# Optimization experiments

Hardware: AMD Instinct MI355X
Metric: run time of the kernel (lower is better)

Reference implementation:

```python
import jax, jax.numpy as jnp
import numpy as np
from jax import lax

B, C, H, W = 32, 256, 56, 56

def _conv(x, w, stride, groups=1, pad='VALID'):
    return lax.conv_general_dilated(x, w, (stride, stride), pad,
                                    feature_group_count=groups,
                                    dimension_numbers=('NCHW', 'OIHW', 'NCHW'))

def _ln(x, g, b, eps=1e-5):
    mu = jnp.mean(x, -1, keepdims=True)
    var = jnp.mean((x - mu) ** 2, -1, keepdims=True)
    return (x - mu) * lax.rsqrt(var + eps) * g + b

def setup_inputs() -> dict:
    key = jax.random.key(0)
    ks = jax.random.split(key, 16)
    s = 0.02
    Ch = C // 2
    d = {}
    d['x'] = jax.random.normal(ks[0], (B, C, H, W), jnp.float32)
    d['Wq'] = jax.random.normal(ks[1], (C, C), jnp.float32) * s;  d['bq'] = jnp.zeros((C,), jnp.float32)
    d['Wk'] = jax.random.normal(ks[2], (C, C), jnp.float32) * s;  d['bk'] = jnp.zeros((C,), jnp.float32)
    d['Wv'] = jax.random.normal(ks[3], (C, C), jnp.float32) * s;  d['bv'] = jnp.zeros((C,), jnp.float32)
    d['sr1_w'] = jax.random.normal(ks[4], (C, C, 8, 8), jnp.float32) * s; d['sr1_b'] = jnp.zeros((C,), jnp.float32)
    d['ln1_g'] = jnp.ones((C,), jnp.float32); d['ln1_b'] = jnp.zeros((C,), jnp.float32)
    d['sr2_w'] = jax.random.normal(ks[5], (C, C, 4, 4), jnp.float32) * s; d['sr2_b'] = jnp.zeros((C,), jnp.float32)
    d['ln2_g'] = jnp.ones((C,), jnp.float32); d['ln2_b'] = jnp.zeros((C,), jnp.float32)
    d['Wkv1'] = jax.random.normal(ks[6], (C, C), jnp.float32) * s; d['bkv1'] = jnp.zeros((C,), jnp.float32)
    d['Wkv2'] = jax.random.normal(ks[7], (C, C), jnp.float32) * s; d['bkv2'] = jnp.zeros((C,), jnp.float32)
    d['lc1_w'] = jax.random.normal(ks[8], (Ch, 1, 3, 3), jnp.float32) * s; d['lc1_b'] = jnp.zeros((Ch,), jnp.float32)
    d['lc2_w'] = jax.random.normal(ks[9], (Ch, 1, 3, 3), jnp.float32) * s; d['lc2_b'] = jnp.zeros((Ch,), jnp.float32)
    d['rp_w'] = jax.random.normal(ks[10], (C, C), jnp.float32) * s;  d['rp_b'] = jnp.zeros((C,), jnp.float32)
    d['rp12_w'] = jax.random.normal(ks[11], (C, C), jnp.float32) * s; d['rp12_b'] = jnp.zeros((C,), jnp.float32)
    d['dw_w'] = jax.random.normal(ks[12], (C, 2), jnp.float32) * 0.5  # Conv3d (2,1,1) depthwise, no bias
    return d

def reference(x, Wq, bq, Wk, bk, Wv, bv, sr1_w, sr1_b, ln1_g, ln1_b,
              sr2_w, sr2_b, ln2_g, ln2_b, Wkv1, bkv1, Wkv2, bkv2,
              lc1_w, lc1_b, lc2_w, lc2_b, rp_w, rp_b, rp12_w, rp12_b, dw_w):
    Bx, Cc, h, w = x.shape
    N = h * w
    Ch = Cc // 2
    xt = x.reshape(Bx, Cc, N).transpose(0, 2, 1)                 # [B,N,C]
    q = jax.nn.softmax(xt @ Wq + bq, axis=-1)                    # softmax over channels
    q1, q2 = q[..., :Ch], q[..., Ch:]

    # spatial-reduction branches (conv -> LN -> GELU)
    x1 = _conv(x, sr1_w, 8) + sr1_b[:, None, None]               # [B,C,7,7]
    x1 = jax.nn.gelu(_ln(x1.reshape(Bx, Cc, -1).transpose(0, 2, 1), ln1_g, ln1_b), approximate=False)
    x2 = _conv(x, sr2_w, 4) + sr2_b[:, None, None]               # [B,C,14,14]
    x2 = jax.nn.gelu(_ln(x2.reshape(Bx, Cc, -1).transpose(0, 2, 1), ln2_g, ln2_b), approximate=False)

    def branch(xr, Wkv, bkv, lc_w, lc_b, qh, hh):
        kv = (xr @ Wkv + bkv).reshape(Bx, -1, 2, Ch)
        k = jax.nn.softmax(kv[:, :, 0], axis=1)                  # softmax over reduced tokens
        v = kv[:, :, 1]
        vsp = v.transpose(0, 2, 1).reshape(Bx, Ch, hh, hh)
        v = v + (_conv(vsp, lc_w, 1, groups=Ch, pad='SAME') + lc_b[:, None, None]).reshape(Bx, Ch, -1).transpose(0, 2, 1)
        ctx = jnp.einsum('bnk,bnv->bkv', k, v)                   # [B,Ch,Ch]
        return jnp.einsum('bnk,bkv->bnv', qh, ctx)               # [B,N,Ch]

    a1 = branch(x1, Wkv1, bkv1, lc1_w, lc1_b, q1, 7)
    a2 = branch(x2, Wkv2, bkv2, lc2_w, lc2_b, q2, 14)
    eff2 = jnp.concatenate([a1, a2], axis=-1)                    # [B,N,C]
    eff2 = jnp.einsum('bni,oi->bon', eff2, rp12_w).reshape(Bx, Cc, h, w) + rp12_b[None, :, None, None]

    # global efficient-attention branch
    keys = jax.nn.softmax(xt @ Wk + bk, axis=1)                  # softmax over tokens
    values = xt @ Wv + bv
    ctx = jnp.einsum('bnk,bnv->bkv', keys, values)               # [B,C,C]
    att = jnp.einsum('bnk,bkv->bnv', q, ctx)                     # [B,N,C]
    eff = jnp.einsum('bni,oi->bon', att, rp_w).reshape(Bx, Cc, h, w) + rp_b[None, :, None, None]

    # Conv3d (2,1,1) depthwise merge over the two branches
    out = eff * dw_w[:, 0][None, :, None, None] + eff2 * dw_w[:, 1][None, :, None, None]
    return out
```

## Files before the change

### kernel.cpp

```cpp
#include <hip/hip_runtime.h>
#include <hip/hip_bf16.h>
#include <math.h>

#define B_ 32
#define H_ 56
#define W_ 56
#define N_ 3136
#define NT_ 100352

typedef short short8 __attribute__((ext_vector_type(8)));
typedef float f32x4 __attribute__((ext_vector_type(4)));

__device__ __forceinline__ unsigned short f2b(float f){
  union { float f; unsigned u; } v; v.f = f;
  return (unsigned short)((v.u + 0x7FFFu + ((v.u>>16)&1u)) >> 16);
}

#define LDSW(row, bo) ((unsigned)((row)*128 + ((bo) ^ (((row)&7)<<4))))

__device__ __forceinline__ short8 ldfrag(const char* base, int row, int kk){
  return *(const short8*)(base + LDSW(row, kk*2));
}
__device__ __forceinline__ f32x4 mfma16(short8 a, short8 b, f32x4 c){
  return __builtin_amdgcn_mfma_f32_16x16x32_bf16(a, b, c, 0, 0, 0);
}

__device__ __forceinline__ void gld16(void* lds, const void* g){
  __builtin_amdgcn_global_load_lds((__attribute__((address_space(1))) void*)g,
                                   (__attribute__((address_space(3))) void*)lds,
                                   16, 0, 0);
}

__global__ void prep_kernel(const float* __restrict__ Wq, const float* __restrict__ Wk,
                            const float* __restrict__ Wv, const float* __restrict__ Wkv1,
                            const float* __restrict__ Wkv2, const float* __restrict__ sr1w,
                            const float* __restrict__ sr2w, const float* __restrict__ rpw,
                            const float* __restrict__ rpb, const float* __restrict__ rp12w,
                            const float* __restrict__ rp12b, const float* __restrict__ dww,
                            unsigned short* WqT, unsigned short* WkT, unsigned short* WvT,
                            unsigned short* Wkv1T, unsigned short* Wkv2T,
                            unsigned short* srw1, unsigned short* srw2,
                            unsigned short* Acomb, float* bias_out)
{
  int idx = blockIdx.x*256 + threadIdx.x;
  const int total = 5*65536 + 4194304 + 1048576 + 131072 + 256;
  for (int i = idx; i < total; i += gridDim.x*256) {
    int j = i;
    if (j < 5*65536) {
      int w = j >> 16, e = j & 65535;
      int o = e >> 8, c = e & 255;
      const float* src = (w==0)?Wq:(w==1)?Wk:(w==2)?Wv:(w==3)?Wkv1:Wkv2;
      unsigned short* dst = (w==0)?WqT:(w==1)?WkT:(w==2)?WvT:(w==3)?Wkv1T:Wkv2T;
      dst[o*256+c] = f2b(src[c*256+o]);
      continue;
    }
    j -= 5*65536;
    if (j < 4194304) {
      int o = j >> 14, rem = j & 16383, pos = rem >> 8, c = rem & 255;
      srw1[j] = f2b(sr1w[o*16384 + c*64 + pos]);
      continue;
    }
    j -= 4194304;
    if (j < 1048576) {
      int o = j >> 12, rem = j & 4095, pos = rem >> 8, c = rem & 255;
      srw2[j] = f2b(sr2w[o*4096 + c*16 + pos]);
      continue;
    }
    j -= 1048576;
    if (j < 131072) {
      int o = j >> 9, i2 = j & 511;
      float v = (i2 < 256) ? dww[o*2+0]*rpw[o*256+i2]
                           : dww[o*2+1]*rp12w[o*256+(i2-256)];
      Acomb[o*512+i2] = f2b(v);
      continue;
    }
    j -= 131072;
    bias_out[j] = dww[j*2+0]*rpb[j] + dww[j*2+1]*rp12b[j];
  }
}

__global__ void transpose_kernel(const float* __restrict__ x, unsigned short* __restrict__ xt)
{
  __shared__ float tile[64][65];
  int bn = blockIdx.x; int b = bn / 49; int n0 = (bn - b*49)*64;
  int c0 = blockIdx.y*64;
  int t = threadIdx.x;
  {
    int cl = t >> 2, nq = t & 3;
    const float* src = x + ((size_t)(b*256 + c0 + cl))*N_ + n0 + nq*16;
#pragma unroll
    for (int j = 0; j < 4; j++){
      float4 v = *(const float4*)(src + j*4);
      tile[cl][nq*16 + j*4 + 0] = v.x;
      tile[cl][nq*16 + j*4 + 1] = v.y;
      tile[cl][nq*16 + j*4 + 2] = v.z;
      tile[cl][nq*16 + j*4 + 3] = v.w;
    }
  }
  __syncthreads();
  {
    int nl = t >> 2, cq = t & 3;
    unsigned short pk[16];
#pragma unroll
    for (int j=0;j<16;j++) pk[j] = f2b(tile[cq*16+j][nl]);
    unsigned short* dst = xt + ((size_t)(b*N_ + n0 + nl))*256 + c0 + cq*16;
    *(uint4*)dst = *(uint4*)&pk[0];
    *(uint4*)(dst+8) = *(uint4*)&pk[8];
  }
}

__global__ __launch_bounds__(256,2) void qkv3_kernel(
    const unsigned short* __restrict__ xt,
    const unsigned short* __restrict__ WqT, const unsigned short* __restrict__ WkT,
    const unsigned short* __restrict__ WvT,
    const float* __restrict__ bq, const float* __restrict__ bk, const float* __restrict__ bv,
    unsigned short* __restrict__ qbuf, unsigned short* __restrict__ KexpT,
    unsigned short* __restrict__ VT, float* __restrict__ s_q, float* __restrict__ s_k)
{
  __shared__ __align__(16) char smem[32768 + 32768 + 1024];
  char* At = smem;
  char* Bt = smem + 32768;
  float* redbuf = (float*)(smem + 65536);
  const int t = threadIdx.x, wave = t>>6, lane = t&63, l15 = lane&15, l4 = lane>>4;
  const int r0 = blockIdx.x*64;
  const int b = r0 / N_;
  const int nl0 = r0 - b*N_;

#pragma unroll
  for (int c4=0;c4<4;c4++)
#pragma unroll
    for (int j=0;j<2;j++){
      int chunk = j*256 + t; int row = chunk>>3, c8 = chunk&7;
      int c8s = c8 ^ (row&7);
      gld16(At + c4*8192 + (j*256 + wave*64)*16,
            xt + (size_t)(r0+row)*256 + c4*64 + c8s*8);
    }
  __syncthreads();

  for (int mat=0; mat<3; mat++){
    const unsigned short* BT = (mat==0)?WqT:(mat==1)?WkT:WvT;
    const float* bias = (mat==0)?bq:(mat==1)?bk:bv;
    const f32x4 vzero = {0.f,0.f,0.f,0.f};
    f32x4 acc[4][4];
#pragma unroll
    for (int i=0;i<4;i++)
#pragma unroll
      for (int j=0;j<4;j++) acc[i][j] = vzero;

    for (int k0c=0;k0c<4;k0c++){
#pragma unroll
      for (int j=0;j<8;j++){
        int chunk = j*256 + t; int row = chunk>>3, c8 = chunk&7;
        int c8s = c8 ^ (row&7);
        gld16(Bt + (j*256 + wave*64)*16, BT + (size_t)row*256 + k0c*64 + c8s*8);
      }
      __syncthreads();
#pragma unroll
      for (int ks=0;ks<2;ks++){
        short8 af[4], bfr[4];
#pragma unroll
        for (int mi=0;mi<4;mi++) af[mi]  = ldfrag(At + k0c*8192, mi*16 + l15, ks*32 + l4*8);
#pragma unroll
        for (int ni=0;ni<4;ni++) bfr[ni] = ldfrag(Bt, wave*64 + ni*16 + l15, ks*32 + l4*8);
#pragma unroll
        for (int mi=0;mi<4;mi++)
#pragma unroll
          for (int ni=0;ni<4;ni++)
            acc[mi][ni] = mfma16(af[mi], bfr[ni], acc[mi][ni]);
      }
      __syncthreads();
    }

    float bb4[4];
#pragma unroll
    for (int ni=0;ni<4;ni++) bb4[ni] = bias[wave*64 + ni*16 + l15];

    if (mat == 0) {
      float rs[4][4];
#pragma unroll
      for (int mi=0;mi<4;mi++)
#pragma unroll
        for (int r=0;r<4;r++) rs[mi][r] = 0.f;
#pragma unroll
      for (int mi=0;mi<4;mi++)
#pragma unroll
        for (int ni=0;ni<4;ni++)
#pragma unroll
          for (int r=0;r<4;r++){
            float e = __expf(acc[mi][ni][r] + bb4[ni]);
            acc[mi][ni][r] = e;
            rs[mi][r] += e;
          }
#pragma unroll
      for (int mi=0;mi<4;mi++)
#pragma unroll
        for (int r=0;r<4;r++){
          float s = rs[mi][r];
          s += __shfl_xor(s, 1); s += __shfl_xor(s, 2);
          s += __shfl_xor(s, 4); s += __shfl_xor(s, 8);
          rs[mi][r] = s;
        }
      if (l15 == 0){
#pragma unroll
        for (int mi=0;mi<4;mi++)
#pragma unroll
          for (int r=0;r<4;r++)
            redbuf[wave*64 + mi*16 + l4*4 + r] = rs[mi][r];
      }
      __syncthreads();
      unsigned short* qb = (unsigned short*)Bt;
#pragma unroll
      for (int mi=0;mi<4;mi++)
#pragma unroll
        for (int r=0;r<4;r++){
          int rr = mi*16 + l4*4 + r;
#pragma unroll
          for (int ni=0;ni<4;ni++)
            qb[rr*256 + wave*64 + ni*16 + l15] = f2b(acc[mi][ni][r]);
        }
      if (t < 64){
        s_q[r0 + t] = redbuf[t] + redbuf[64+t] + redbuf[128+t] + redbuf[192+t];
      }
      __syncthreads();
#pragma unroll
      for (int j=0;j<8;j++){
        int chunk = j*256 + t;
        int row = chunk >> 5, c8 = chunk & 31;
        *(uint4*)(qbuf + (size_t)(r0+row)*256 + c8*8) = *(const uint4*)(qb + row*256 + c8*8);
      }
      __syncthreads();
    } else {
      float cs[4] = {0.f,0.f,0.f,0.f};
#pragma unroll
      for (int mi=0;mi<4;mi++)
#pragma unroll
        for (int ni=0;ni<4;ni++)
#pragma unroll
          for (int r=0;r<4;r++){
            float v = acc[mi][ni][r] + bb4[ni];
            if (mat == 1){ v = __expf(v); cs[ni] += v; }
            int row = mi*16 + l4*4 + r;
            int col = wave*64 + ni*16 + l15;
            *(unsigned short*)(Bt + LDSW(col, row*2)) = f2b(v);
          }
      if (mat == 1){
#pragma unroll
        for (int ni=0;ni<4;ni++){
          float s = cs[ni];
          s += __shfl_xor(s, 16);
          s += __shfl_xor(s, 32);
          if (lane < 16) atomicAdd(&s_k[b*256 + wave*64 + ni*16 + lane], s);
        }
      }
      __syncthreads();
      unsigned short* ot = (mat==1) ? KexpT : VT;
#pragma unroll
      for (int j=0;j<8;j++){
        int chunk = j*256 + t;
        int c = chunk >> 3, n8 = chunk & 7;
        *(uint4*)(ot + ((size_t)b*256 + c)*N_ + nl0 + n8*8) = *(const uint4*)(Bt + LDSW(c, n8*16));
      }
      __syncthreads();
    }
  }
}

template<int MODE>
__global__ __launch_bounds__(256,2) void tile128_kernel(
    const unsigned short* __restrict__ Ag, const unsigned short* __restrict__ Bg,
    unsigned short* __restrict__ outg, float* __restrict__ part)
{
  __shared__ __align__(16) char smem[32768];
  char* At = smem; char* Bt = smem + 16384;
  const int b = blockIdx.x;
  const int mt = (MODE==0) ? (blockIdx.y >> 1) : blockIdx.y;
  const int nt = (MODE==0) ? (blockIdx.y & 1)  : blockIdx.z;
  const int it0 = (MODE==0) ? blockIdx.z*7 : 0;
  const int it1 = (MODE==0) ? it0+7 : 8;
  const int t = threadIdx.x;
  const int wave = t>>6, lane = t&63, l15 = lane&15, l4 = lane>>4;
  const int wm = (wave>>1)*64, wn = (wave&1)*64;
  const size_t astr = (MODE==0) ? (size_t)N_ : (size_t)512;
  const unsigned short* A  = (MODE==0) ? (Ag + ((size_t)b*256 + mt*128)*N_) : (Ag + (size_t)mt*128*512);
  const unsigned short* Bv = (MODE==0) ? (Bg + ((size_t)b*256 + nt*128)*N_) : (Bg + ((size_t)b*256 + nt*128)*512);
  const f32x4 vzero = {0.f,0.f,0.f,0.f};
  f32x4 acc[4][4];
#pragma unroll
  for (int i=0;i<4;i++)
#pragma unroll
    for (int j=0;j<4;j++) acc[i][j] = vzero;

  for (int it=it0; it<it1; it++){
    const int k0 = it*64;
#pragma unroll
    for (int j=0;j<4;j++){
      int chunk = j*256 + t; int row = chunk>>3, c8 = chunk&7;
      int c8s = c8 ^ (row&7);
      gld16(At + (j*256 + wave*64)*16, A + (size_t)row*astr + k0 + c8s*8);
    }
#pragma unroll
    for (int j=0;j<4;j++){
      int chunk = j*256 + t; int row = chunk>>3, c8 = chunk&7;
      int c8s = c8 ^ (row&7);
      gld16(Bt + (j*256 + wave*64)*16, Bv + (size_t)row*astr + k0 + c8s*8);
    }
    __syncthreads();
#pragma unroll
    for (int ks=0;ks<2;ks++){
      short8 af[4], bfr[4];
#pragma unroll
      for (int mi=0;mi<4;mi++) af[mi]  = ldfrag(At, wm + mi*16 + l15, ks*32 + l4*8);
#pragma unroll
      for (int ni=0;ni<4;ni++) bfr[ni] = ldfrag(Bt, wn + ni*16 + l15, ks*32 + l4*8);
#pragma unroll
      for (int mi=0;mi<4;mi++)
#pragma unroll
        for (int ni=0;ni<4;ni++)
          acc[mi][ni] = mfma16(af[mi], bfr[ni], acc[mi][ni]);
    }
    __syncthreads();
  }
  if (MODE==0){
    const int sk = blockIdx.z;
#pragma unroll
    for (int mi=0;mi<4;mi++)
#pragma unroll
      for (int r=0;r<4;r++){
        int kg = mt*128 + wm + mi*16 + l4*4 + r;
        size_t basep = (((size_t)sk*B_ + b)*256 + kg)*256 + nt*128 + wn;
#pragma unroll
        for (int ni=0;ni<4;ni++)
          part[basep + ni*16 + l15] = acc[mi][ni][r];
      }
  } else {
#pragma unroll
    for (int mi=0;mi<4;mi++)
#pragma unroll
      for (int r=0;r<4;r++){
        int og = mt*128 + wm + mi*16 + l4*4 + r;
#pragma unroll
        for (int ni=0;ni<4;ni++)
          outg[(size_t)b*65536 + (size_t)og*256 + nt*128 + wn + ni*16 + l15] = f2b(acc[mi][ni][r]);
      }
  }
}

__global__ __launch_bounds__(256) void ctxred_kernel(
    const float* __restrict__ part, const float* __restrict__ s_k,
    unsigned short* __restrict__ ctxcomb)
{
  int e = (blockIdx.x*256 + threadIdx.x)*4;
  int b = e >> 16; int rem = e & 65535; int kg = rem >> 8; int col = rem & 255;
  float4 s = {0.f,0.f,0.f,0.f};
#pragma unroll
  for (int sk=0; sk<7; sk++){
    float4 p = *(const float4*)(part + ((((size_t)sk*B_ + b)*256 + kg)<<8) + col);
    s.x += p.x; s.y += p.y; s.z += p.z; s.w += p.w;
  }
  float inv = 1.0f / s_k[b*256 + kg];
  unsigned short pk[4] = {f2b(s.x*inv), f2b(s.y*inv), f2b(s.z*inv), f2b(s.w*inv)};
  *(uint2*)(ctxcomb + ((size_t)b*256 + kg)*512 + col) = *(uint2*)&pk[0];
}

template<int S, int OW, int KW, int NSK, int MPB, int KTOT>
__device__ __forceinline__ void srconv_body(
    const unsigned short* __restrict__ xt, const unsigned short* __restrict__ wbf,
    float* __restrict__ part, int bid, char* At, char* Bt)
{
  const int KCH = KTOT / NSK;
  const int Mtot = B_*MPB;
  const int sk = bid % NSK, tile = bid / NSK;
  const int t = threadIdx.x, wave = t>>6, lane = t&63, l15 = lane&15, l4 = lane>>4;
  const f32x4 vzero = {0.f,0.f,0.f,0.f};
  f32x4 acc[4][4];
#pragma unroll
  for (int i=0;i<4;i++)
#pragma unroll
    for (int j=0;j<4;j++) acc[i][j] = vzero;

  size_t abase[2];
#pragma unroll
  for (int j=0;j<2;j++){
    int chunk = j*256 + t;
    int row = chunk >> 3, c8 = chunk & 7;
    int c8s = c8 ^ (row&7);
    int rowc = tile*64 + row; if (rowc > Mtot-1) rowc = Mtot-1;
    int b = rowc / MPB; int m = rowc - b*MPB;
    int p = m / OW; int q = m - p*OW;
    abase[j] = ((size_t)b*N_ + (size_t)(S*p)*W_ + S*q)*256 + c8s*8;
  }

  for (int kt = 0; kt < KCH; kt += 64){
    const int k0 = sk*KCH + kt;
    const int pos = k0 >> 8, cc = k0 & 255;
    const int dy = pos / KW, dx = pos - dy*KW;
    const size_t off = (size_t)(dy*W_ + dx)*256 + cc;
#pragma unroll
    for (int j=0;j<2;j++){
      gld16(At + (j*256 + wave*64)*16, xt + abase[j] + off);
    }
#pragma unroll
    for (int j=0;j<8;j++){
      int chunk = j*256 + t; int row = chunk>>3, c8 = chunk&7;
      int c8s = c8 ^ (row&7);
      gld16(Bt + (j*256 + wave*64)*16, wbf + (size_t)row*KTOT + k0 + c8s*8);
    }
    __syncthreads();
#pragma unroll
    for (int ks=0;ks<2;ks++){
      short8 af[4], bfr[4];
#pragma unroll
      for (int mi=0;mi<4;mi++) af[mi]  = ldfrag(At, mi*16 + l15, ks*32 + l4*8);
#pragma unroll
      for (int ni=0;ni<4;ni++) bfr[ni] = ldfrag(Bt, wave*64 + ni*16 + l15, ks*32 + l4*8);
#pragma unroll
      for (int mi=0;mi<4;mi++)
#pragma unroll
        for (int ni=0;ni<4;ni++)
          acc[mi][ni] = mfma16(af[mi], bfr[ni], acc[mi][ni]);
    }
    __syncthreads();
  }
#pragma unroll
  for (int mi=0;mi<4;mi++)
#pragma unroll
    for (int r=0;r<4;r++){
      int row = tile*64 + mi*16 + l4*4 + r;
      if (row < Mtot){
        size_t basep = ((size_t)sk*Mtot + row)*256;
#pragma unroll
        for (int ni=0;ni<4;ni++)
          part[basep + wave*64 + ni*16 + l15] = acc[mi][ni][r];
      }
    }
}

__global__ __launch_bounds__(256,4) void srconv_both_kernel(
    const unsigned short* __restrict__ xt, const unsigned short* __restrict__ srw1,
    const unsigned short* __restrict__ srw2, float* __restrict__ x1part,
    float* __restrict__ x2part)
{
  __shared__ __align__(16) char smem[8192 + 32768];
  if (blockIdx.x < 392)
    srconv_body<4,14,4,4,196,4096>(xt, srw2, x2part, blockIdx.x, smem, smem+8192);
  else
    srconv_body<8,7,8,32,49,16384>(xt, srw1, x1part, blockIdx.x-392, smem, smem+8192);
}

__device__ __forceinline__ void lngelu_body(
    const float* __restrict__ part, const float* __restrict__ srb,
    const float* __restrict__ g, const float* __restrict__ bb,
    unsigned short* __restrict__ out, int M, int nsk, int Mtot, int bid,
    float* red)
{
  int b = bid / M, m = bid - b*M;
  int c = threadIdx.x;
  float v = srb[c];
  for (int s=0;s<nsk;s++) v += part[((size_t)s*Mtot + b*M + m)*256 + c];
  int wave = c>>6, lane = c&63;
  float s1 = v;
  s1 += __shfl_xor(s1,1); s1 += __shfl_xor(s1,2); s1 += __shfl_xor(s1,4);
  s1 += __shfl_xor(s1,8); s1 += __shfl_xor(s1,16); s1 += __shfl_xor(s1,32);
  if (lane==0) red[wave] = s1;
  __syncthreads();
  float mu = (red[0]+red[1]+red[2]+red[3]) * (1.0f/256.0f);
  float d = v - mu;
  float s2 = d*d;
  s2 += __shfl_xor(s2,1); s2 += __shfl_xor(s2,2); s2 += __shfl_xor(s2,4);
  s2 += __shfl_xor(s2,8); s2 += __shfl_xor(s2,16); s2 += __shfl_xor(s2,32);
  if (lane==0) red[4+wave] = s2;
  __syncthreads();
  float var = (red[4]+red[5]+red[6]+red[7]) * (1.0f/256.0f);
  float y = d * rsqrtf(var + 1e-5f) * g[c] + bb[c];
  float ge = 0.5f * y * (1.0f + erff(y * 0.70710678118654752f));
  out[((size_t)b*M + m)*256 + c] = f2b(ge);
}

__global__ __launch_bounds__(256) void lngelu_both_kernel(
    const float* __restrict__ x1part, const float* __restrict__ x2part,
    const float* __restrict__ sr1b, const float* __restrict__ sr2b,
    const float* __restrict__ ln1g, const float* __restrict__ ln1b,
    const float* __restrict__ ln2g, const float* __restrict__ ln2b,
    unsigned short* __restrict__ x1g, unsigned short* __restrict__ x2g)
{
  __shared__ float red[8];
  if (blockIdx.x < 1568)
    lngelu_body(x1part, sr1b, ln1g, ln1b, x1g, 49, 32, 1568, blockIdx.x, red);
  else
    lngelu_body(x2part, sr2b, ln2g, ln2b, x2g, 196, 4, 6272, blockIdx.x-1568, red);
}

__global__ __launch_bounds__(256,2) void kv_both_kernel(
    const unsigned short* __restrict__ x1g, const unsigned short* __restrict__ Wkv1T,
    const float* __restrict__ bkv1, float* __restrict__ kexp1, float* __restrict__ vraw1,
    const unsigned short* __restrict__ x2g, const unsigned short* __restrict__ Wkv2T,
    const float* __restrict__ bkv2, float* __restrict__ kexp2, float* __restrict__ vraw2)
{
  __shared__ __align__(16) char smem[8192 + 32768];
  char* At = smem; char* Bt = smem + 8192;
  const unsigned short* A; const unsigned short* BT; const float* bias;
  float* kexp; float* vraw; int r0; int R;
  if (blockIdx.x < 25){ A=x1g; BT=Wkv1T; bias=bkv1; kexp=kexp1; vraw=vraw1; r0=blockIdx.x*64; R=1568; }
  else { A=x2g; BT=Wkv2T; bias=bkv2; kexp=kexp2; vraw=vraw2; r0=(blockIdx.x-25)*64; R=6272; }
  const int t = threadIdx.x, wave = t>>6, lane = t&63, l15 = lane&15, l4 = lane>>4;
  const f32x4 vzero = {0.f,0.f,0.f,0.f};
  f32x4 acc[4][4];
#pragma unroll
  for (int i=0;i<4;i++)
#pragma unroll
    for (int j=0;j<4;j++) acc[i][j] = vzero;

  for (int k0 = 0; k0 < 256; k0 += 64) {
#pragma unroll
    for (int j = 0; j < 2; j++){
      int chunk = j*256 + t;
      int row = chunk >> 3, c8 = chunk & 7;
      int c8s = c8 ^ (row&7);
      int rg = r0 + row; if (rg > R-1) rg = R-1;
      gld16(At + (j*256 + wave*64)*16, A + (size_t)rg*256 + k0 + c8s*8);
    }
#pragma unroll
    for (int j = 0; j < 8; j++){
      int chunk = j*256 + t;
      int row = chunk >> 3, c8 = chunk & 7;
      int c8s = c8 ^ (row&7);
      gld16(Bt + (j*256 + wave*64)*16, BT + (size_t)row*256 + k0 + c8s*8);
    }
    __syncthreads();
#pragma unroll
    for (int ks = 0; ks < 2; ks++){
      short8 af[4], bfr[4];
#pragma unroll
      for (int mi=0;mi<4;mi++) af[mi]  = ldfrag(At, mi*16 + l15, ks*32 + l4*8);
#pragma unroll
      for (int ni=0;ni<4;ni++) bfr[ni] = ldfrag(Bt, wave*64 + ni*16 + l15, ks*32 + l4*8);
#pragma unroll
      for (int mi=0;mi<4;mi++)
#pragma unroll
        for (int ni=0;ni<4;ni++)
          acc[mi][ni] = mfma16(af[mi], bfr[ni], acc[mi][ni]);
    }
    __syncthreads();
  }
  float bb4[4];
#pragma unroll
  for (int ni=0;ni<4;ni++) bb4[ni] = bias[wave*64 + ni*16 + l15];
#pragma unroll
  for (int mi=0;mi<4;mi++)
#pragma unroll
    for (int ni=0;ni<4;ni++)
#pragma unroll
      for (int r=0;r<4;r++){
        int rg = r0 + mi*16 + l4*4 + r;
        if (rg < R){
          int col = wave*64 + ni*16 + l15;
          float v = acc[mi][ni][r] + bb4[ni];
          if (col < 128) kexp[(size_t)rg*128 + col] = __expf(v);
          else           vraw[(size_t)rg*128 + (col-128)] = v;
        }
      }
}

__device__ __forceinline__ void dwconv_body(
    const float* __restrict__ vraw, const float* __restrict__ lcw,
    const float* __restrict__ lcb, float* __restrict__ vmod, int M, int OW, int idx)
{
  int ch = idx & 127; int rest = idx >> 7; int m = rest % M; int b = rest / M;
  if (b >= B_) return;
  int py = m / OW, px = m - py*OW;
  float acc = vraw[((size_t)b*M + m)*128 + ch] + lcb[ch];
#pragma unroll
  for (int dy=0;dy<3;dy++)
#pragma unroll
    for (int dx=0;dx<3;dx++){
      int yy = py+dy-1, xx = px+dx-1;
      if (yy>=0 && yy<OW && xx>=0 && xx<OW)
        acc += vraw[((size_t)b*M + yy*OW+xx)*128 + ch] * lcw[ch*9 + dy*3 + dx];
    }
  vmod[((size_t)b*M + m)*128 + ch] = acc;
}

__global__ __launch_bounds__(256) void dwconv_both_kernel(
    const float* __restrict__ vraw1, const float* __restrict__ lc1w,
    const float* __restrict__ lc1b, float* __restrict__ vmod1,
    const float* __restrict__ vraw2, const float* __restrict__ lc2w,
    const float* __restrict__ lc2b, float* __restrict__ vmod2)
{
  int gid = blockIdx.x*256 + threadIdx.x;
  if (blockIdx.x < 784) dwconv_body(vraw1, lc1w, lc1b, vmod1, 49, 7, gid);
  else dwconv_body(vraw2, lc2w, lc2b, vmod2, 196, 14, gid - 784*256);
}

__global__ __launch_bounds__(512) void ctxbr_both_kernel(
    const float* __restrict__ kexp1, const float* __restrict__ vmod1,
    const float* __restrict__ kexp2, const float* __restrict__ vmod2,
    unsigned short* __restrict__ ctxcomb)
{
  const int b = blockIdx.x;
  int kc = blockIdx.y;
  const float* kexp; const float* vmod; int M, BR;
  if (kc < 32){ kexp = kexp1; vmod = vmod1; M = 49; BR = 0; }
  else { kexp = kexp2; vmod = vmod2; M = 196; BR = 1; kc -= 32; }
  const int t = threadIdx.x;
  const int kl = t >> 7, j = t & 127;
  const int kk = kc*4 + kl;
  const float* kp = kexp + (size_t)b*M*128 + kk;
  const float* vp = vmod + (size_t)b*M*128 + j;
  float acc = 0.f, s = 0.f;
  for (int m = 0; m < M; m++){
    float kv = kp[(size_t)m*128];
    s += kv;
    acc += kv * vp[(size_t)m*128];
  }
  const int krow = BR ? (128+kk) : kk;
  unsigned short* dst = ctxcomb + ((size_t)b*256 + krow)*512;
  const int wbase = BR ? 384 : 256;
  const int zbase = BR ? 256 : 384;
  dst[wbase + j] = f2b(acc / s);
  dst[zbase + j] = 0;
}

__global__ __launch_bounds__(256,2) void final_kernel(
    const unsigned short* __restrict__ Gmat, const unsigned short* __restrict__ qbuf,
    const float* __restrict__ bias_out, const float* __restrict__ s_q,
    float* __restrict__ out)
{
  __shared__ __align__(16) char smem[16384 + 8192];
  char* At = smem; char* Bt = smem + 16384;
  const int b = blockIdx.x, ot = blockIdx.y, nt = blockIdx.z;
  const int t = threadIdx.x, wave = t>>6, lane = t&63, l15 = lane&15, l4 = lane>>4;
  const int wm = (wave>>1)*64, wn = (wave&1)*32;
  const unsigned short* A  = Gmat + ((size_t)b*256 + ot*128)*256;
  const unsigned short* Bq = qbuf + ((size_t)b*N_ + nt*64)*256;
  const f32x4 vzero = {0.f,0.f,0.f,0.f};
  f32x4 acc[4][2];
#pragma unroll
  for (int i=0;i<4;i++){ acc[i][0] = vzero; acc[i][1] = vzero; }

  for (int k0=0;k0<256;k0+=64){
#pragma unroll
    for (int j=0;j<4;j++){
      int chunk = j*256 + t; int row = chunk>>3, c8 = chunk&7;
      int c8s = c8 ^ (row&7);
      gld16(At + (j*256 + wave*64)*16, A + (size_t)row*256 + k0 + c8s*8);
    }
#pragma unroll
    for (int j=0;j<2;j++){
      int chunk = j*256 + t; int row = chunk>>3, c8 = chunk&7;
      int c8s = c8 ^ (row&7);
      gld16(Bt + (j*256 + wave*64)*16, Bq + (size_t)row*256 + k0 + c8s*8);
    }
    __syncthreads();
#pragma unroll
    for (int ks=0;ks<2;ks++){
      short8 af[4], bfr[2];
#pragma unroll
      for (int mi=0;mi<4;mi++) af[mi]  = ldfrag(At, wm + mi*16 + l15, ks*32 + l4*8);
#pragma unroll
      for (int ni=0;ni<2;ni++) bfr[ni] = ldfrag(Bt, wn + ni*16 + l15, ks*32 + l4*8);
#pragma unroll
      for (int mi=0;mi<4;mi++)
#pragma unroll
        for (int ni=0;ni<2;ni++)
          acc[mi][ni] = mfma16(af[mi], bfr[ni], acc[mi][ni]);
    }
    __syncthreads();
  }
  float iq[2];
#pragma unroll
  for (int ni=0;ni<2;ni++)
    iq[ni] = 1.0f / s_q[(size_t)b*N_ + nt*64 + wn + ni*16 + l15];
#pragma unroll
  for (int mi=0;mi<4;mi++)
#pragma unroll
    for (int r=0;r<4;r++){
      int o = ot*128 + wm + mi*16 + l4*4 + r;
      float bo = bias_out[o];
#pragma unroll
      for (int ni=0;ni<2;ni++){
        int n = nt*64 + wn + ni*16 + l15;
        out[((size_t)b*256 + o)*N_ + n] = acc[mi][ni][r]*iq[ni] + bo;
      }
    }
}

extern "C" void kernel_launch(void* const* d_in, const int* in_sizes, int n_in,
                              void* d_out, int out_size, void* d_ws, size_t ws_size,
                              hipStream_t stream)
{
  const float* x     = (const float*)d_in[0];
  const float* Wq    = (const float*)d_in[1];
  const float* bq    = (const float*)d_in[2];
  const float* Wk    = (const float*)d_in[3];
  const float* bk    = (const float*)d_in[4];
  const float* Wv    = (const float*)d_in[5];
  const float* bv    = (const float*)d_in[6];
  const float* sr1w  = (const float*)d_in[7];
  const float* sr1b  = (const float*)d_in[8];
  const float* ln1g  = (const float*)d_in[9];
  const float* ln1b  = (const float*)d_in[10];
  const float* sr2w  = (const float*)d_in[11];
  const float* sr2b  = (const float*)d_in[12];
  const float* ln2g  = (const float*)d_in[13];
  const float* ln2b  = (const float*)d_in[14];
  const float* Wkv1  = (const float*)d_in[15];
  const float* bkv1  = (const float*)d_in[16];
  const float* Wkv2  = (const float*)d_in[17];
  const float* bkv2  = (const float*)d_in[18];
  const float* lc1w  = (const float*)d_in[19];
  const float* lc1b  = (const float*)d_in[20];
  const float* lc2w  = (const float*)d_in[21];
  const float* lc2b  = (const float*)d_in[22];
  const float* rpw   = (const float*)d_in[23];
  const float* rpb   = (const float*)d_in[24];
  const float* rp12w = (const float*)d_in[25];
  const float* rp12b = (const float*)d_in[26];
  const float* dww   = (const float*)d_in[27];

  char* ws = (char*)d_ws;
  size_t off = 0;
  auto take = [&](size_t n)->char*{ char* p = ws + off; off += (n + 255) & ~(size_t)255; return p; };

  unsigned short* WqT   = (unsigned short*)take(131072);
  unsigned short* WkT   = (unsigned short*)take(131072);
  unsigned short* WvT   = (unsigned short*)take(131072);
  unsigned short* Wkv1T = (unsigned short*)take(131072);
  unsigned short* Wkv2T = (unsigned short*)take(131072);
  unsigned short* srw1  = (unsigned short*)take(8388608);
  unsigned short* srw2  = (unsigned short*)take(2097152);
  unsigned short* Acomb = (unsigned short*)take(262144);
  float* bias_out = (float*)take(1024);
  float* s_k      = (float*)take(32768);
  float* s_q      = (float*)take(401408);
  char* regionA = take(51380224);
  unsigned short* qbuf = (unsigned short*)take(51380224);
  char* regionK = take(51380224);
  char* regionV = take(51380224);
  if (off > ws_size) return;

  unsigned short* xt    = (unsigned short*)regionA;
  unsigned short* KexpT = (unsigned short*)regionK;
  float* x1part = (float*)regionK;
  unsigned short* VT = (unsigned short*)regionV;
  unsigned short* Gmat = (unsigned short*)regionV;
  unsigned short* x1g  = (unsigned short*)(regionV + 4194304);
  unsigned short* x2g  = (unsigned short*)(regionV + 4997120);
  float* x2part = (float*)(regionV + 8208384);
  float* kexp1 = (float*)(regionV + 8208384);
  float* vraw1 = (float*)(regionV + 9011200);
  float* vmod1 = (float*)(regionV + 9814016);
  float* kexp2 = (float*)(regionV + 10616832);
  float* vraw2 = (float*)(regionV + 13828096);
  float* vmod2 = (float*)(regionV + 17039360);
  unsigned short* ctxcomb = (unsigned short*)d_out;
  float* ctxpart = (float*)((char*)d_out + 8388608);

  hipMemsetAsync(s_k, 0, 32768, stream);
  prep_kernel<<<8192, 256, 0, stream>>>(Wq, Wk, Wv, Wkv1, Wkv2, sr1w, sr2w,
                                        rpw, rpb, rp12w, rp12b, dww,
                                        WqT, WkT, WvT, Wkv1T, Wkv2T, srw1, srw2,
                                        Acomb, bias_out);
  transpose_kernel<<<dim3(1568,4), 256, 0, stream>>>(x, xt);
  qkv3_kernel<<<1568, 256, 0, stream>>>(xt, WqT, WkT, WvT, bq, bk, bv,
                                        qbuf, KexpT, VT, s_q, s_k);
  tile128_kernel<0><<<dim3(32,4,7), 256, 0, stream>>>(KexpT, VT, nullptr, ctxpart);
  ctxred_kernel<<<2048, 256, 0, stream>>>(ctxpart, s_k, ctxcomb);
  srconv_both_kernel<<<1192, 256, 0, stream>>>(xt, srw1, srw2, x1part, x2part);
  lngelu_both_kernel<<<7840, 256, 0, stream>>>(x1part, x2part, sr1b, sr2b,
                                               ln1g, ln1b, ln2g, ln2b, x1g, x2g);
  kv_both_kernel<<<123, 256, 0, stream>>>(x1g, Wkv1T, bkv1, kexp1, vraw1,
                                          x2g, Wkv2T, bkv2, kexp2, vraw2);
  dwconv_both_kernel<<<3920, 256, 0, stream>>>(vraw1, lc1w, lc1b, vmod1,
                                               vraw2, lc2w, lc2b, vmod2);
  ctxbr_both_kernel<<<dim3(32,64), 512, 0, stream>>>(kexp1, vmod1, kexp2, vmod2, ctxcomb);
  tile128_kernel<1><<<dim3(32,2,2), 256, 0, stream>>>(Acomb, ctxcomb, Gmat, nullptr);
  final_kernel<<<dim3(32,2,49), 256, 0, stream>>>(Gmat, qbuf, bias_out, s_q, (float*)d_out);
}
```

Measured before the change: 424.5 us.

## Double-buffer weight tiles in qkv kernel and swizzle q staging buffer

The QKV projection kernel now stages weight K-chunks of 32 into two LDS ping-pong buffers with a new packed, XOR-swizzled layout, so the load of the next chunk overlaps MFMA work on the current one. This halves the barriers per chunk and removes the load-then-wait stall of the previous loop. The q staging writes and reads through LDS are also XOR-swizzled to cut bank conflicts. The cost is more complex address arithmetic, and the initial barrier after the A load is removed, so correctness relies on the barrier after the first B stage.

```diff
diff --git a/kernel.cpp b/kernel.cpp
--- a/kernel.cpp
+++ b/kernel.cpp
@@ -109,7 +109,7 @@
   }
 }
 
-__global__ __launch_bounds__(256,2) void qkv3_kernel(
+__global__ __launch_bounds__(256,2) void qkv4_kernel(
     const unsigned short* __restrict__ xt,
     const unsigned short* __restrict__ WqT, const unsigned short* __restrict__ WkT,
     const unsigned short* __restrict__ WvT,
@@ -135,7 +135,17 @@
       gld16(At + c4*8192 + (j*256 + wave*64)*16,
             xt + (size_t)(r0+row)*256 + c4*64 + c8s*8);
     }
-  __syncthreads();
+
+  auto stageB = [&](char* dst, const unsigned short* BT, int kc){
+#pragma unroll
+    for (int j=0;j<4;j++){
+      int s = j*256 + t;
+      int p = s>>3, o = s&7;
+      unsigned u = (unsigned)((o*16) ^ ((p&7)<<4));
+      gld16(dst + (j*256 + wave*64)*16,
+            BT + (size_t)(p*2 + (u>>6))*256 + kc*32 + ((u&63)>>1));
+    }
+  };
 
   for (int mat=0; mat<3; mat++){
     const unsigned short* BT = (mat==0)?WqT:(mat==1)?WkT:WvT;
@@ -147,27 +157,28 @@
 #pragma unroll
       for (int j=0;j<4;j++) acc[i][j] = vzero;
 
-    for (int k0c=0;k0c<4;k0c++){
-#pragma unroll
-      for (int j=0;j<8;j++){
-        int chunk = j*256 + t; int row = chunk>>3, c8 = chunk&7;
-        int c8s = c8 ^ (row&7);
-        gld16(Bt + (j*256 + wave*64)*16, BT + (size_t)row*256 + k0c*64 + c8s*8);
-      }
-      __syncthreads();
-#pragma unroll
-      for (int ks=0;ks<2;ks++){
-        short8 af[4], bfr[4];
-#pragma unroll
-        for (int mi=0;mi<4;mi++) af[mi]  = ldfrag(At + k0c*8192, mi*16 + l15, ks*32 + l4*8);
-#pragma unroll
-        for (int ni=0;ni<4;ni++) bfr[ni] = ldfrag(Bt, wave*64 + ni*16 + l15, ks*32 + l4*8);
-#pragma unroll
-        for (int mi=0;mi<4;mi++)
-#pragma unroll
-          for (int ni=0;ni<4;ni++)
-            acc[mi][ni] = mfma16(af[mi], bfr[ni], acc[mi][ni]);
-      }
+    stageB(Bt, BT, 0);
+    __syncthreads();
+
+    for (int kc=0; kc<8; kc++){
+      char* cur = Bt + (kc&1)*16384;
+      if (kc < 7) stageB(Bt + ((kc+1)&1)*16384, BT, kc+1);
+      short8 af[4], bfr[4];
+#pragma unroll
+      for (int mi=0;mi<4;mi++)
+        af[mi] = ldfrag(At + (kc>>1)*8192, mi*16 + l15, (kc&1)*32 + l4*8);
+#pragma unroll
+      for (int ni=0;ni<4;ni++){
+        int c = wave*64 + ni*16 + l15;
+        int p = c>>1;
+        unsigned off = (unsigned)((((c&1)*64) + l4*16) ^ ((p&7)<<4));
+        bfr[ni] = *(const short8*)(cur + p*128 + off);
+      }
+#pragma unroll
+      for (int mi=0;mi<4;mi++)
+#pragma unroll
+        for (int ni=0;ni<4;ni++)
+          acc[mi][ni] = mfma16(af[mi], bfr[ni], acc[mi][ni]);
       __syncthreads();
     }
 
@@ -215,8 +226,11 @@
         for (int r=0;r<4;r++){
           int rr = mi*16 + l4*4 + r;
 #pragma unroll
-          for (int ni=0;ni<4;ni++)
-            qb[rr*256 + wave*64 + ni*16 + l15] = f2b(acc[mi][ni][r]);
+          for (int ni=0;ni<4;ni++){
+            int col = wave*64 + ni*16 + l15;
+            unsigned bo = (unsigned)((col*2) ^ ((rr&7)<<4));
+            *(unsigned short*)((char*)qb + rr*512 + bo) = f2b(acc[mi][ni][r]);
+          }
         }
       if (t < 64){
         s_q[r0 + t] = redbuf[t] + redbuf[64+t] + redbuf[128+t] + redbuf[192+t];
@@ -226,7 +240,8 @@
       for (int j=0;j<8;j++){
         int chunk = j*256 + t;
         int row = chunk >> 5, c8 = chunk & 31;
-        *(uint4*)(qbuf + (size_t)(r0+row)*256 + c8*8) = *(const uint4*)(qb + row*256 + c8*8);
+        unsigned bo = (unsigned)((c8*16) ^ ((row&7)<<4));
+        *(uint4*)(qbuf + (size_t)(r0+row)*256 + c8*8) = *(const uint4*)((char*)qb + row*512 + bo);
       }
       __syncthreads();
     } else {
@@ -761,7 +776,7 @@
                                         WqT, WkT, WvT, Wkv1T, Wkv2T, srw1, srw2,
                                         Acomb, bias_out);
   transpose_kernel<<<dim3(1568,4), 256, 0, stream>>>(x, xt);
-  qkv3_kernel<<<1568, 256, 0, stream>>>(xt, WqT, WkT, WvT, bq, bk, bv,
+  qkv4_kernel<<<1568, 256, 0, stream>>>(xt, WqT, WkT, WvT, bq, bk, bv,
                                         qbuf, KexpT, VT, s_q, s_k);
   tile128_kernel<0><<<dim3(32,4,7), 256, 0, stream>>>(KexpT, VT, nullptr, ctxpart);
   ctxred_kernel<<<2048, 256, 0, stream>>>(ctxpart, s_k, ctxcomb);
```

Measured after the change: 434.5 us. 1.02x slower.

## Merge global ctx GEMM into the SR-conv launch and ctx reduction into LN

Applied to the files above, without the earlier changes.

Runs the global-branch KexpT·V context GEMM as extra blocks inside the spatial-reduction conv kernel, and the split-K context reduction as extra blocks inside the LayerNorm/GELU kernel. This removes two launches and lets independent work share the same wave of blocks. The sr1 conv split-K drops from 32 to 16 so the block counts fit together. x1part and x2part move to separate buffers because KexpT/VT must stay alive while the conv runs. The ctx blocks now use a 4-block-per-CU launch bound instead of 2, which may cause register spilling.

```diff
diff --git a/kernel.cpp b/kernel.cpp
--- a/kernel.cpp
+++ b/kernel.cpp
@@ -24,7 +24,6 @@
 __device__ __forceinline__ f32x4 mfma16(short8 a, short8 b, f32x4 c){
   return __builtin_amdgcn_mfma_f32_16x16x32_bf16(a, b, c, 0, 0, 0);
 }
-
 __device__ __forceinline__ void gld16(void* lds, const void* g){
   __builtin_amdgcn_global_load_lds((__attribute__((address_space(1))) void*)g,
                                    (__attribute__((address_space(3))) void*)lds,
@@ -265,103 +264,6 @@
   }
 }
 
-template<int MODE>
-__global__ __launch_bounds__(256,2) void tile128_kernel(
-    const unsigned short* __restrict__ Ag, const unsigned short* __restrict__ Bg,
-    unsigned short* __restrict__ outg, float* __restrict__ part)
-{
-  __shared__ __align__(16) char smem[32768];
-  char* At = smem; char* Bt = smem + 16384;
-  const int b = blockIdx.x;
-  const int mt = (MODE==0) ? (blockIdx.y >> 1) : blockIdx.y;
-  const int nt = (MODE==0) ? (blockIdx.y & 1)  : blockIdx.z;
-  const int it0 = (MODE==0) ? blockIdx.z*7 : 0;
-  const int it1 = (MODE==0) ? it0+7 : 8;
-  const int t = threadIdx.x;
-  const int wave = t>>6, lane = t&63, l15 = lane&15, l4 = lane>>4;
-  const int wm = (wave>>1)*64, wn = (wave&1)*64;
-  const size_t astr = (MODE==0) ? (size_t)N_ : (size_t)512;
-  const unsigned short* A  = (MODE==0) ? (Ag + ((size_t)b*256 + mt*128)*N_) : (Ag + (size_t)mt*128*512);
-  const unsigned short* Bv = (MODE==0) ? (Bg + ((size_t)b*256 + nt*128)*N_) : (Bg + ((size_t)b*256 + nt*128)*512);
-  const f32x4 vzero = {0.f,0.f,0.f,0.f};
-  f32x4 acc[4][4];
-#pragma unroll
-  for (int i=0;i<4;i++)
-#pragma unroll
-    for (int j=0;j<4;j++) acc[i][j] = vzero;
-
-  for (int it=it0; it<it1; it++){
-    const int k0 = it*64;
-#pragma unroll
-    for (int j=0;j<4;j++){
-      int chunk = j*256 + t; int row = chunk>>3, c8 = chunk&7;
-      int c8s = c8 ^ (row&7);
-      gld16(At + (j*256 + wave*64)*16, A + (size_t)row*astr + k0 + c8s*8);
-    }
-#pragma unroll
-    for (int j=0;j<4;j++){
-      int chunk = j*256 + t; int row = chunk>>3, c8 = chunk&7;
-      int c8s = c8 ^ (row&7);
-      gld16(Bt + (j*256 + wave*64)*16, Bv + (size_t)row*astr + k0 + c8s*8);
-    }
-    __syncthreads();
-#pragma unroll
-    for (int ks=0;ks<2;ks++){
-      short8 af[4], bfr[4];
-#pragma unroll
-      for (int mi=0;mi<4;mi++) af[mi]  = ldfrag(At, wm + mi*16 + l15, ks*32 + l4*8);
-#pragma unroll
-      for (int ni=0;ni<4;ni++) bfr[ni] = ldfrag(Bt, wn + ni*16 + l15, ks*32 + l4*8);
-#pragma unroll
-      for (int mi=0;mi<4;mi++)
-#pragma unroll
-        for (int ni=0;ni<4;ni++)
-          acc[mi][ni] = mfma16(af[mi], bfr[ni], acc[mi][ni]);
-    }
-    __syncthreads();
-  }
-  if (MODE==0){
-    const int sk = blockIdx.z;
-#pragma unroll
-    for (int mi=0;mi<4;mi++)
-#pragma unroll
-      for (int r=0;r<4;r++){
-        int kg = mt*128 + wm + mi*16 + l4*4 + r;
-        size_t basep = (((size_t)sk*B_ + b)*256 + kg)*256 + nt*128 + wn;
-#pragma unroll
-        for (int ni=0;ni<4;ni++)
-          part[basep + ni*16 + l15] = acc[mi][ni][r];
-      }
-  } else {
-#pragma unroll
-    for (int mi=0;mi<4;mi++)
-#pragma unroll
-      for (int r=0;r<4;r++){
-        int og = mt*128 + wm + mi*16 + l4*4 + r;
-#pragma unroll
-        for (int ni=0;ni<4;ni++)
-          outg[(size_t)b*65536 + (size_t)og*256 + nt*128 + wn + ni*16 + l15] = f2b(acc[mi][ni][r]);
-      }
-  }
-}
-
-__global__ __launch_bounds__(256) void ctxred_kernel(
-    const float* __restrict__ part, const float* __restrict__ s_k,
-    unsigned short* __restrict__ ctxcomb)
-{
-  int e = (blockIdx.x*256 + threadIdx.x)*4;
-  int b = e >> 16; int rem = e & 65535; int kg = rem >> 8; int col = rem & 255;
-  float4 s = {0.f,0.f,0.f,0.f};
-#pragma unroll
-  for (int sk=0; sk<7; sk++){
-    float4 p = *(const float4*)(part + ((((size_t)sk*B_ + b)*256 + kg)<<8) + col);
-    s.x += p.x; s.y += p.y; s.z += p.z; s.w += p.w;
-  }
-  float inv = 1.0f / s_k[b*256 + kg];
-  unsigned short pk[4] = {f2b(s.x*inv), f2b(s.y*inv), f2b(s.z*inv), f2b(s.w*inv)};
-  *(uint2*)(ctxcomb + ((size_t)b*256 + kg)*512 + col) = *(uint2*)&pk[0];
-}
-
 template<int S, int OW, int KW, int NSK, int MPB, int KTOT>
 __device__ __forceinline__ void srconv_body(
     const unsigned short* __restrict__ xt, const unsigned short* __restrict__ wbf,
@@ -435,16 +337,81 @@
     }
 }
 
-__global__ __launch_bounds__(256,4) void srconv_both_kernel(
+__device__ __forceinline__ void ctxmain_body(
+    const unsigned short* __restrict__ KexpT, const unsigned short* __restrict__ VT,
+    float* __restrict__ part, int idx, char* At, char* Bt)
+{
+  const int b = idx / 28; int rem = idx - b*28;
+  const int y = rem / 7, sk = rem - y*7;
+  const int mt = y >> 1, nt = y & 1;
+  const int it0 = sk*7, it1 = it0+7;
+  const int t = threadIdx.x;
+  const int wave = t>>6, lane = t&63, l15 = lane&15, l4 = lane>>4;
+  const int wm = (wave>>1)*64, wn = (wave&1)*64;
+  const unsigned short* A  = KexpT + ((size_t)b*256 + mt*128)*N_;
+  const unsigned short* Bv = VT + ((size_t)b*256 + nt*128)*N_;
+  const f32x4 vzero = {0.f,0.f,0.f,0.f};
+  f32x4 acc[4][4];
+#pragma unroll
+  for (int i=0;i<4;i++)
+#pragma unroll
+    for (int j=0;j<4;j++) acc[i][j] = vzero;
+
+  for (int it=it0; it<it1; it++){
+    const int k0 = it*64;
+#pragma unroll
+    for (int j=0;j<4;j++){
+      int chunk = j*256 + t; int row = chunk>>3, c8 = chunk&7;
+      int c8s = c8 ^ (row&7);
+      gld16(At + (j*256 + wave*64)*16, A + (size_t)row*N_ + k0 + c8s*8);
+    }
+#pragma unroll
+    for (int j=0;j<4;j++){
+      int chunk = j*256 + t; int row = chunk>>3, c8 = chunk&7;
+      int c8s = c8 ^ (row&7);
+      gld16(Bt + (j*256 + wave*64)*16, Bv + (size_t)row*N_ + k0 + c8s*8);
+    }
+    __syncthreads();
+#pragma unroll
+    for (int ks=0;ks<2;ks++){
+      short8 af[4], bfr[4];
+#pragma unroll
+      for (int mi=0;mi<4;mi++) af[mi]  = ldfrag(At, wm + mi*16 + l15, ks*32 + l4*8);
+#pragma unroll
+      for (int ni=0;ni<4;ni++) bfr[ni] = ldfrag(Bt, wn + ni*16 + l15, ks*32 + l4*8);
+#pragma unroll
+      for (int mi=0;mi<4;mi++)
+#pragma unroll
+        for (int ni=0;ni<4;ni++)
+          acc[mi][ni] = mfma16(af[mi], bfr[ni], acc[mi][ni]);
+    }
+    __syncthreads();
+  }
+#pragma unroll
+  for (int mi=0;mi<4;mi++)
+#pragma unroll
+    for (int r=0;r<4;r++){
+      int kg = mt*128 + wm + mi*16 + l4*4 + r;
+      size_t basep = (((size_t)sk*B_ + b)*256 + kg)*256 + nt*128 + wn;
+#pragma unroll
+      for (int ni=0;ni<4;ni++)
+        part[basep + ni*16 + l15] = acc[mi][ni][r];
+    }
+}
+
+__global__ __launch_bounds__(256,4) void conv_ctx_kernel(
     const unsigned short* __restrict__ xt, const unsigned short* __restrict__ srw1,
     const unsigned short* __restrict__ srw2, float* __restrict__ x1part,
-    float* __restrict__ x2part)
+    float* __restrict__ x2part, const unsigned short* __restrict__ KexpT,
+    const unsigned short* __restrict__ VT, float* __restrict__ ctxpart)
 {
   __shared__ __align__(16) char smem[8192 + 32768];
   if (blockIdx.x < 392)
     srconv_body<4,14,4,4,196,4096>(xt, srw2, x2part, blockIdx.x, smem, smem+8192);
+  else if (blockIdx.x < 792)
+    srconv_body<8,7,8,16,49,16384>(xt, srw1, x1part, blockIdx.x-392, smem, smem+8192);
   else
-    srconv_body<8,7,8,32,49,16384>(xt, srw1, x1part, blockIdx.x-392, smem, smem+8192);
+    ctxmain_body(KexpT, VT, ctxpart, blockIdx.x-792, smem, smem+16384);
 }
 
 __device__ __forceinline__ void lngelu_body(
@@ -476,18 +443,93 @@
   out[((size_t)b*M + m)*256 + c] = f2b(ge);
 }
 
-__global__ __launch_bounds__(256) void lngelu_both_kernel(
+__global__ __launch_bounds__(256) void red_ln_kernel(
     const float* __restrict__ x1part, const float* __restrict__ x2part,
     const float* __restrict__ sr1b, const float* __restrict__ sr2b,
     const float* __restrict__ ln1g, const float* __restrict__ ln1b,
     const float* __restrict__ ln2g, const float* __restrict__ ln2b,
-    unsigned short* __restrict__ x1g, unsigned short* __restrict__ x2g)
+    unsigned short* __restrict__ x1g, unsigned short* __restrict__ x2g,
+    const float* __restrict__ ctxpart, const float* __restrict__ s_k,
+    unsigned short* __restrict__ ctxcomb)
 {
   __shared__ float red[8];
-  if (blockIdx.x < 1568)
-    lngelu_body(x1part, sr1b, ln1g, ln1b, x1g, 49, 32, 1568, blockIdx.x, red);
-  else
+  if (blockIdx.x < 1568){
+    lngelu_body(x1part, sr1b, ln1g, ln1b, x1g, 49, 16, 1568, blockIdx.x, red);
+  } else if (blockIdx.x < 7840){
     lngelu_body(x2part, sr2b, ln2g, ln2b, x2g, 196, 4, 6272, blockIdx.x-1568, red);
+  } else {
+    int e = ((blockIdx.x-7840)*256 + threadIdx.x)*4;
+    int b = e >> 16; int rem = e & 65535; int kg = rem >> 8; int col = rem & 255;
+    float4 s = {0.f,0.f,0.f,0.f};
+#pragma unroll
+    for (int sk=0; sk<7; sk++){
+      float4 p = *(const float4*)(ctxpart + ((((size_t)sk*B_ + b)*256 + kg)<<8) + col);
+      s.x += p.x; s.y += p.y; s.z += p.z; s.w += p.w;
+    }
+    float inv = 1.0f / s_k[b*256 + kg];
+    unsigned short pk[4] = {f2b(s.x*inv), f2b(s.y*inv), f2b(s.z*inv), f2b(s.w*inv)};
+    *(uint2*)(ctxcomb + ((size_t)b*256 + kg)*512 + col) = *(uint2*)&pk[0];
+  }
+}
+
+__global__ __launch_bounds__(256,2) void gmat_kernel(
+    const unsigned short* __restrict__ Acomb, const unsigned short* __restrict__ ctxcomb,
+    unsigned short* __restrict__ outg)
+{
+  __shared__ __align__(16) char smem[32768];
+  char* At = smem; char* Bt = smem + 16384;
+  const int b = blockIdx.x, mt = blockIdx.y, nt = blockIdx.z;
+  const int t = threadIdx.x;
+  const int wave = t>>6, lane = t&63, l15 = lane&15, l4 = lane>>4;
+  const int wm = (wave>>1)*64, wn = (wave&1)*64;
+  const unsigned short* A  = Acomb + (size_t)mt*128*512;
+  const unsigned short* Bv = ctxcomb + ((size_t)b*256 + nt*128)*512;
+  const f32x4 vzero = {0.f,0.f,0.f,0.f};
+  f32x4 acc[4][4];
+#pragma unroll
+  for (int i=0;i<4;i++)
+#pragma unroll
+    for (int j=0;j<4;j++) acc[i][j] = vzero;
+
+  for (int it=0; it<8; it++){
+    const int k0 = it*64;
+#pragma unroll
+    for (int j=0;j<4;j++){
+      int chunk = j*256 + t; int row = chunk>>3, c8 = chunk&7;
+      int c8s = c8 ^ (row&7);
+      gld16(At + (j*256 + wave*64)*16, A + (size_t)row*512 + k0 + c8s*8);
+    }
+#pragma unroll
+    for (int j=0;j<4;j++){
+      int chunk = j*256 + t; int row = chunk>>3, c8 = chunk&7;
+      int c8s = c8 ^ (row&7);
+      gld16(Bt + (j*256 + wave*64)*16, Bv + (size_t)row*512 + k0 + c8s*8);
+    }
+    __syncthreads();
+#pragma unroll
+    for (int ks=0;ks<2;ks++){
+      short8 af[4], bfr[4];
+#pragma unroll
+      for (int mi=0;mi<4;mi++) af[mi]  = ldfrag(At, wm + mi*16 + l15, ks*32 + l4*8);
+#pragma unroll
+      for (int ni=0;ni<4;ni++) bfr[ni] = ldfrag(Bt, wn + ni*16 + l15, ks*32 + l4*8);
+#pragma unroll
+      for (int mi=0;mi<4;mi++)
+#pragma unroll
+        for (int ni=0;ni<4;ni++)
+          acc[mi][ni] = mfma16(af[mi], bfr[ni], acc[mi][ni]);
+    }
+    __syncthreads();
+  }
+#pragma unroll
+  for (int mi=0;mi<4;mi++)
+#pragma unroll
+    for (int r=0;r<4;r++){
+      int og = mt*128 + wm + mi*16 + l4*4 + r;
+#pragma unroll
+      for (int ni=0;ni<4;ni++)
+        outg[(size_t)b*65536 + (size_t)og*256 + nt*128 + wn + ni*16 + l15] = f2b(acc[mi][ni][r]);
+    }
 }
 
 __global__ __launch_bounds__(256,2) void kv_both_kernel(
@@ -736,16 +778,15 @@
   unsigned short* qbuf = (unsigned short*)take(51380224);
   char* regionK = take(51380224);
   char* regionV = take(51380224);
+  float* x1part = (float*)take(25690112);
   if (off > ws_size) return;
 
   unsigned short* xt    = (unsigned short*)regionA;
   unsigned short* KexpT = (unsigned short*)regionK;
-  float* x1part = (float*)regionK;
   unsigned short* VT = (unsigned short*)regionV;
   unsigned short* Gmat = (unsigned short*)regionV;
   unsigned short* x1g  = (unsigned short*)(regionV + 4194304);
   unsigned short* x2g  = (unsigned short*)(regionV + 4997120);
-  float* x2part = (float*)(regionV + 8208384);
   float* kexp1 = (float*)(regionV + 8208384);
   float* vraw1 = (float*)(regionV + 9011200);
   float* vmod1 = (float*)(regionV + 9814016);
@@ -754,6 +795,7 @@
   float* vmod2 = (float*)(regionV + 17039360);
   unsigned short* ctxcomb = (unsigned short*)d_out;
   float* ctxpart = (float*)((char*)d_out + 8388608);
+  float* x2part  = (float*)((char*)d_out + 67108864);
 
   hipMemsetAsync(s_k, 0, 32768, stream);
   prep_kernel<<<8192, 256, 0, stream>>>(Wq, Wk, Wv, Wkv1, Wkv2, sr1w, sr2w,
@@ -763,16 +805,16 @@
   transpose_kernel<<<dim3(1568,4), 256, 0, stream>>>(x, xt);
   qkv3_kernel<<<1568, 256, 0, stream>>>(xt, WqT, WkT, WvT, bq, bk, bv,
                                         qbuf, KexpT, VT, s_q, s_k);
-  tile128_kernel<0><<<dim3(32,4,7), 256, 0, stream>>>(KexpT, VT, nullptr, ctxpart);
-  ctxred_kernel<<<2048, 256, 0, stream>>>(ctxpart, s_k, ctxcomb);
-  srconv_both_kernel<<<1192, 256, 0, stream>>>(xt, srw1, srw2, x1part, x2part);
-  lngelu_both_kernel<<<7840, 256, 0, stream>>>(x1part, x2part, sr1b, sr2b,
-                                               ln1g, ln1b, ln2g, ln2b, x1g, x2g);
+  conv_ctx_kernel<<<392+400+896, 256, 0, stream>>>(xt, srw1, srw2,
+                                                   x1part, x2part, KexpT, VT, ctxpart);
+  red_ln_kernel<<<7840+2048, 256, 0, stream>>>(x1part, x2part, sr1b, sr2b,
+                                               ln1g, ln1b, ln2g, ln2b, x1g, x2g,
+                                               ctxpart, s_k, ctxcomb);
   kv_both_kernel<<<123, 256, 0, stream>>>(x1g, Wkv1T, bkv1, kexp1, vraw1,
                                           x2g, Wkv2T, bkv2, kexp2, vraw2);
   dwconv_both_kernel<<<3920, 256, 0, stream>>>(vraw1, lc1w, lc1b, vmod1,
                                                vraw2, lc2w, lc2b, vmod2);
   ctxbr_both_kernel<<<dim3(32,64), 512, 0, stream>>>(kexp1, vmod1, kexp2, vmod2, ctxcomb);
-  tile128_kernel<1><<<dim3(32,2,2), 256, 0, stream>>>(Acomb, ctxcomb, Gmat, nullptr);
+  gmat_kernel<<<dim3(32,2,2), 256, 0, stream>>>(Acomb, ctxcomb, Gmat);
   final_kernel<<<dim3(32,2,49), 256, 0, stream>>>(Gmat, qbuf, bias_out, s_q, (float*)d_out);
 }
```

New measurement: 424.0 us. Within noise of the previous version (-0.1%).
